# Kernel tuning notes

Measured on AMD Instinct MI355X. Metric: run time of the kernel, lower is better.

Reference implementation:

```python
import jax, jax.numpy as jnp
import numpy as np

N = 50000
E = 800000
IN_C = 256
OUT_C = 256
HEADS = 8
HEAD_C = OUT_C // HEADS  # 32
BNECK = OUT_C // 4       # 64
NEG_SLOPE = 0.2
BN_EPS = 1e-5


def _bn(x, gamma, beta):
    # BatchNorm1d over node dim, batch statistics (deterministic train-mode math)
    mu = jnp.mean(x, axis=0)
    var = jnp.var(x, axis=0)
    return (x - mu) * jax.lax.rsqrt(var + BN_EPS) * gamma + beta


def setup_inputs() -> dict:
    key = jax.random.key(0)
    ks = jax.random.split(key, 16)
    s = lambda fan: 1.0 / np.sqrt(fan)
    x = jax.random.normal(ks[0], (N, IN_C), dtype=jnp.float32)
    edge_index = jax.random.randint(ks[1], (2, E), 0, N, dtype=jnp.int64)
    return {
        "x": x,
        "edge_index": edge_index,
        # GATConv params (lin has no bias in PyG)
        "W_lin": jax.random.normal(ks[2], (IN_C, HEADS * HEAD_C), jnp.float32) * s(IN_C),
        "att_src": jax.random.normal(ks[3], (HEADS, HEAD_C), jnp.float32) * s(HEAD_C),
        "att_dst": jax.random.normal(ks[4], (HEADS, HEAD_C), jnp.float32) * s(HEAD_C),
        "conv_bias": jnp.zeros((HEADS * HEAD_C,), jnp.float32),
        "W_res": jax.random.normal(ks[5], (IN_C, HEADS * HEAD_C), jnp.float32) * s(IN_C),
        # gnn.BatchNorm
        "g_norm": jnp.ones((OUT_C,), jnp.float32),
        "b_norm": jnp.zeros((OUT_C,), jnp.float32),
        # Bottleneck down
        "W_down": jax.random.normal(ks[6], (OUT_C, BNECK), jnp.float32) * s(OUT_C),
        "b_down": jnp.zeros((BNECK,), jnp.float32),
        "g_down": jnp.ones((BNECK,), jnp.float32),
        "bb_down": jnp.zeros((BNECK,), jnp.float32),
        # Bottleneck up
        "W_up": jax.random.normal(ks[7], (BNECK, OUT_C), jnp.float32) * s(BNECK),
        "b_up": jnp.zeros((OUT_C,), jnp.float32),
        "g_up": jnp.ones((OUT_C,), jnp.float32),
        "bb_up": jnp.zeros((OUT_C,), jnp.float32),
    }


def _forward(x, edge_index, W_lin, att_src, att_dst, conv_bias, W_res,
             g_norm, b_norm, W_down, b_down, g_down, bb_down,
             W_up, b_up, g_up, bb_up):
    src, dst = edge_index[0], edge_index[1]
    # --- GATConv ---
    xh = (x @ W_lin).reshape(N, HEADS, HEAD_C)            # [N,H,C]
    a_src = jnp.einsum("nhc,hc->nh", xh, att_src)          # [N,H]
    a_dst = jnp.einsum("nhc,hc->nh", xh, att_dst)          # [N,H]
    e = a_src[src] + a_dst[dst]                             # [E,H]
    e = jnp.where(e > 0, e, NEG_SLOPE * e)                  # leaky_relu
    # segment softmax over destination nodes (numerically stable)
    m = jax.ops.segment_max(e, dst, num_segments=N)         # [N,H]
    m = jnp.where(jnp.isfinite(m), m, 0.0)
    ex = jnp.exp(e - m[dst])
    denom = jax.ops.segment_sum(ex, dst, num_segments=N)    # [N,H]
    alpha = ex / (denom[dst] + 1e-16)                        # [E,H]
    msgs = xh[src] * alpha[:, :, None]                       # [E,H,C]
    out = jax.ops.segment_sum(msgs, dst, num_segments=N)    # [N,H,C]
    out = out.reshape(N, HEADS * HEAD_C) + conv_bias + x @ W_res  # GAT residual + bias
    # --- norm + act ---
    h = jax.nn.elu(_bn(out, g_norm, b_norm))
    # --- bottleneck ---
    d = jax.nn.elu(_bn(h @ W_down + b_down, g_down, bb_down))
    u = jax.nn.elu(_bn(d @ W_up + b_up, g_up, bb_up))
    h = h + u
    # dropout: eval mode (identity); in==out so identity skip
    return h + x


def reference(x, edge_index, W_lin, att_src, att_dst, conv_bias, W_res,
              g_norm, b_norm, W_down, b_down, g_down, bb_down,
              W_up, b_up, g_up, bb_up):
    return _forward(x, edge_index, W_lin, att_src, att_dst, conv_bias, W_res,
                    g_norm, b_norm, W_down, b_down, g_down, bb_down,
                    W_up, b_up, g_up, bb_up)
```

## Files before the change

### kernel.cpp

```cpp
#include <hip/hip_runtime.h>

#define NN 50000
#define EE 800000
#define HEADS 8
#define NEG 0.2f
#define BN_EPS 1e-5f
#define SCAN_B 196
#define STAT_B 64

typedef unsigned int uint;
typedef unsigned short ushort;

typedef __bf16 bf16x8 __attribute__((ext_vector_type(8)));
typedef float f32x4 __attribute__((ext_vector_type(4)));

__device__ __forceinline__ float bflo(uint u) { return __uint_as_float(u << 16); }
__device__ __forceinline__ float bfhi(uint u) { return __uint_as_float(u & 0xffff0000u); }
__device__ __forceinline__ float bf1(ushort u) { return __uint_as_float(((uint)u) << 16); }
__device__ __forceinline__ ushort f2bf(float f) {
  uint u = __float_as_uint(f);
  u += 0x7fff + ((u >> 16) & 1);
  return (ushort)(u >> 16);
}
__device__ __forceinline__ uint pk2(float a, float b) {
  return (uint)f2bf(a) | ((uint)f2bf(b) << 16);
}
__device__ __forceinline__ float eluf(float v) { return v > 0.f ? v : expm1f(v); }

__global__ void k_detect(const uint* __restrict__ xw, const int* __restrict__ ew,
                         int* __restrict__ flags) {
  int l = threadIdx.x;
  int good = 0, zeros = 0;
#pragma unroll
  for (int j = 0; j < 4; ++j) {
    uint lo = xw[l * 4 + j] & 0xffffu;
    uint ex = (lo >> 7) & 0xffu;
    good += (ex >= 110u && ex <= 140u) ? 1 : 0;
    zeros += (ew[2 * (l * 4 + j) + 1] == 0) ? 1 : 0;
  }
  for (int o = 32; o; o >>= 1) { good += __shfl_down(good, o); zeros += __shfl_down(zeros, o); }
  if (l == 0) { flags[0] = (good >= 128) ? 1 : 0; flags[1] = (zeros >= 200) ? 1 : 0; }
}

__global__ void k_params(const void* p0, const void* p1, const void* p2, const void* p3,
                         const void* p4, const void* p5, const void* p6, const void* p7,
                         const void* p8, const void* p9, const void* p10,
                         float* __restrict__ P, const int* __restrict__ flags) {
  const void* srcs[11] = {p0, p1, p2, p3, p4, p5, p6, p7, p8, p9, p10};
  const int sz[11]  = {256, 256, 256, 256, 256, 64, 64, 64, 256, 256, 256};
  const int off[11] = {0, 256, 512, 768, 1024, 1280, 1344, 1408, 1472, 1728, 1984};
  int b = blockIdx.x, t = threadIdx.x;
  if (t < sz[b]) {
    const void* s = srcs[b];
    float v = flags[0] ? bf1(((const ushort*)s)[t]) : ((const float*)s)[t];
    P[off[b] + t] = v;
  }
}

__global__ void k_transpose(const void* __restrict__ src, ushort* __restrict__ dst,
                            int R, int C, int D, const int* __restrict__ flags) {
  __shared__ ushort tile[64][65];
  int r0 = blockIdx.x * 64, c0 = blockIdx.y * 64;
  int t = threadIdx.x;
  int tr = t >> 6;
  int tc = t & 63;
  int bf = flags[0];
#pragma unroll
  for (int i = 0; i < 16; ++i) {
    int rl = tr + i * 4;
    int r = r0 + rl, c = c0 + tc;
    float v = 0.f;
    if (r < R && c < C)
      v = bf ? bf1(((const ushort*)src)[(size_t)r * C + c])
             : ((const float*)src)[(size_t)r * C + c];
    tile[rl][tc] = f2bf(v);
  }
  __syncthreads();
#pragma unroll
  for (int i = 0; i < 16; ++i) {
    int cl = tr + i * 4;
    int rl = tc;
    int c = c0 + cl, r = r0 + rl;
    if (c < D && r < R)
      dst[(size_t)c * R + r] = (c < C) ? tile[rl][cl] : (ushort)0;
  }
}

__global__ void k_edges(const int* __restrict__ raw, int* __restrict__ sc, int* __restrict__ dc,
                        int* __restrict__ count, const int* __restrict__ flags) {
  int e = blockIdx.x * 256 + threadIdx.x;
  if (e >= EE) return;
  int s, d;
  if (flags[1]) { s = raw[2 * e]; d = raw[2 * (EE + e)]; }
  else          { s = raw[e];     d = raw[EE + e]; }
  if ((uint)s >= NN) s = 0;
  if ((uint)d >= NN) d = 0;
  sc[e] = s; dc[e] = d;
  atomicAdd(&count[d], 1);
}

__global__ __launch_bounds__(256)
void k_gemm(const void* __restrict__ A, const ushort* __restrict__ Bt,
            const int* __restrict__ flags, int aMode,
            int M, int K, int mode,
            ushort* __restrict__ o_xh, ushort* __restrict__ o_xres,
            ushort* __restrict__ o_bf, int NC, const float* __restrict__ bias) {
  __shared__ __align__(16) ushort As[128 * 32];
  __shared__ __align__(16) ushort Bs[128 * 32];
  int t = threadIdx.x;
  int l = t & 63, w = t >> 6;
  int wr = w >> 1, wc = w & 1;
  int lr = l & 15, lq = l >> 4;
  int m0 = blockIdx.y * 128;
  int n0 = blockIdx.x * 128;
  const int af32 = (aMode == 1) && (flags[0] == 0);
  const ushort* Ab = (const ushort*)A;
  const float*  Af = (const float*)A;

  f32x4 acc[4][4];
#pragma unroll
  for (int i = 0; i < 4; ++i)
#pragma unroll
    for (int j = 0; j < 4; ++j) acc[i][j] = (f32x4){0.f, 0.f, 0.f, 0.f};

  for (int kt = 0; kt < K; kt += 32) {
    __syncthreads();
#pragma unroll
    for (int r = 0; r < 2; ++r) {
      int ci = r * 256 + t;
      int m = ci >> 2, ko = (ci & 3) << 3;
      int gm = m0 + m; gm = gm < M ? gm : M - 1;
      if (af32) {
        float4 u0 = *(const float4*)(Af + (size_t)gm * K + kt + ko);
        float4 u1 = *(const float4*)(Af + (size_t)gm * K + kt + ko + 4);
        uint4 o;
        o.x = pk2(u0.x, u0.y); o.y = pk2(u0.z, u0.w);
        o.z = pk2(u1.x, u1.y); o.w = pk2(u1.z, u1.w);
        *(uint4*)(&As[m * 32 + ko]) = o;
      } else {
        *(uint4*)(&As[m * 32 + ko]) = *(const uint4*)(Ab + (size_t)gm * K + kt + ko);
      }
      *(uint4*)(&Bs[m * 32 + ko]) = *(const uint4*)(Bt + (size_t)(n0 + m) * K + kt + ko);
    }
    __syncthreads();
    bf16x8 af[4], bf[4];
#pragma unroll
    for (int i = 0; i < 4; ++i) {
      af[i] = *(const bf16x8*)(&As[(wr * 64 + i * 16 + lr) * 32 + lq * 8]);
      bf[i] = *(const bf16x8*)(&Bs[(wc * 64 + i * 16 + lr) * 32 + lq * 8]);
    }
#pragma unroll
    for (int i = 0; i < 4; ++i)
#pragma unroll
      for (int j = 0; j < 4; ++j)
        acc[i][j] = __builtin_amdgcn_mfma_f32_16x16x32_bf16(af[i], bf[j], acc[i][j], 0, 0, 0);
  }

#pragma unroll
  for (int i = 0; i < 4; ++i) {
    int gr0 = m0 + wr * 64 + i * 16 + lq * 4;
#pragma unroll
    for (int j = 0; j < 4; ++j) {
      int gc = n0 + wc * 64 + j * 16 + lr;
#pragma unroll
      for (int r = 0; r < 4; ++r) {
        int row = gr0 + r;
        if (row >= M) continue;
        float v = acc[i][j][r];
        if (mode == 0) {
          if (gc < 256) o_xh[(size_t)row * 256 + gc] = f2bf(v);
          else          o_xres[(size_t)row * 256 + (gc - 256)] = f2bf(v);
        } else {
          if (gc < NC) o_bf[(size_t)row * NC + gc] = f2bf(v + bias[gc]);
        }
      }
    }
  }
}

__global__ void k_attn(const ushort* __restrict__ xh, const float* __restrict__ P,
                       float* __restrict__ a_src, float* __restrict__ a_dst) {
  int id = blockIdx.x * 256 + threadIdx.x;
  if (id >= NN * HEADS) return;
  int n = id >> 3, h = id & 7;
  const uint4* xr = (const uint4*)(xh + (size_t)n * 256 + h * 32);
  const float4* pa = (const float4*)(P + h * 32);
  const float4* pd = (const float4*)(P + 256 + h * 32);
  float s = 0.f, d = 0.f;
#pragma unroll
  for (int j = 0; j < 4; ++j) {
    uint4 q = xr[j];
    float4 a0 = pa[2 * j], a1 = pa[2 * j + 1];
    float4 d0 = pd[2 * j], d1 = pd[2 * j + 1];
    float x0 = bflo(q.x), x1 = bfhi(q.x), x2 = bflo(q.y), x3 = bfhi(q.y);
    float x4 = bflo(q.z), x5 = bfhi(q.z), x6 = bflo(q.w), x7 = bfhi(q.w);
    s += x0 * a0.x + x1 * a0.y + x2 * a0.z + x3 * a0.w
       + x4 * a1.x + x5 * a1.y + x6 * a1.z + x7 * a1.w;
    d += x0 * d0.x + x1 * d0.y + x2 * d0.z + x3 * d0.w
       + x4 * d1.x + x5 * d1.y + x6 * d1.z + x7 * d1.w;
  }
  a_src[id] = s; a_dst[id] = d;
}

__global__ void k_scan_bs(const int* __restrict__ count, int* __restrict__ bsum) {
  __shared__ int s[256];
  int i = blockIdx.x * 256 + threadIdx.x;
  s[threadIdx.x] = (i < NN) ? count[i] : 0;
  __syncthreads();
  for (int off = 128; off > 0; off >>= 1) {
    if (threadIdx.x < off) s[threadIdx.x] += s[threadIdx.x + off];
    __syncthreads();
  }
  if (threadIdx.x == 0) bsum[blockIdx.x] = s[0];
}

__global__ void k_scan_top(const int* __restrict__ bsum, int* __restrict__ boff,
                           int* __restrict__ rowptr) {
  __shared__ int s[256];
  int t = threadIdx.x;
  int v = (t < SCAN_B) ? bsum[t] : 0;
  s[t] = v;
  __syncthreads();
  for (int off = 1; off < 256; off <<= 1) {
    int u = (t >= off) ? s[t - off] : 0;
    __syncthreads();
    s[t] += u;
    __syncthreads();
  }
  boff[t] = s[t] - v;
  if (t == 255) rowptr[NN] = s[255];
}

__global__ void k_scan_wr(const int* __restrict__ count, const int* __restrict__ boff,
                          int* __restrict__ rowptr, int* __restrict__ rowwork) {
  __shared__ int s[256];
  int b = blockIdx.x, t = threadIdx.x;
  int i = b * 256 + t;
  int v = (i < NN) ? count[i] : 0;
  s[t] = v;
  __syncthreads();
  for (int off = 1; off < 256; off <<= 1) {
    int u = (t >= off) ? s[t - off] : 0;
    __syncthreads();
    s[t] += u;
    __syncthreads();
  }
  if (i < NN) {
    int ex = boff[b] + s[t] - v;
    rowptr[i] = ex;
    rowwork[i] = ex;
  }
}

__global__ void k_scatter(const int* __restrict__ sc, const int* __restrict__ dc,
                          int* __restrict__ rowwork, int* __restrict__ perm_src) {
  int e = blockIdx.x * 256 + threadIdx.x;
  if (e >= EE) return;
  int pos = atomicAdd(&rowwork[dc[e]], 1);
  perm_src[pos] = sc[e];
}

__global__ __launch_bounds__(256)
void k_aggregate(const int* __restrict__ rowptr, const int* __restrict__ perm_src,
                 const float* __restrict__ a_src, const float* __restrict__ a_dst,
                 const ushort* __restrict__ xh, const ushort* __restrict__ xres,
                 const float* __restrict__ bias, ushort* __restrict__ outb) {
  int n = blockIdx.x * 4 + (threadIdx.x >> 6);
  int l = threadIdx.x & 63;
  if (n >= NN) return;
  int half = l >> 5;
  int q = l & 31;
  int h = q >> 2;
  float ad = a_dst[n * 8 + h];
  int st = rowptr[n], en = rowptr[n + 1];
  float a0 = 0.f, a1 = 0.f, a2 = 0.f, a3 = 0.f;
  float a4 = 0.f, a5 = 0.f, a6 = 0.f, a7 = 0.f, sum = 0.f;
  int p = st + half;
  int s_c = 0; float e_c = 0.f; uint4 x_c = {0, 0, 0, 0};
  if (p < en) {
    s_c = perm_src[p];
    e_c = a_src[s_c * 8 + h];
    x_c = *(const uint4*)(xh + (size_t)s_c * 256 + q * 8);
  }
  for (; p < en; p += 2) {
    int pn = p + 2;
    int s_n = 0; float e_n = 0.f; uint4 x_n = {0, 0, 0, 0};
    if (pn < en) {
      s_n = perm_src[pn];
      e_n = a_src[s_n * 8 + h];
      x_n = *(const uint4*)(xh + (size_t)s_n * 256 + q * 8);
    }
    float v = e_c + ad;
    v = v > 0.f ? v : NEG * v;
    float wgt = __expf(fminf(v, 60.f));
    sum += wgt;
    a0 += wgt * bflo(x_c.x); a1 += wgt * bfhi(x_c.x);
    a2 += wgt * bflo(x_c.y); a3 += wgt * bfhi(x_c.y);
    a4 += wgt * bflo(x_c.z); a5 += wgt * bfhi(x_c.z);
    a6 += wgt * bflo(x_c.w); a7 += wgt * bfhi(x_c.w);
    s_c = s_n; e_c = e_n; x_c = x_n;
  }
  sum += __shfl_xor(sum, 32);
  a0 += __shfl_xor(a0, 32); a1 += __shfl_xor(a1, 32);
  a2 += __shfl_xor(a2, 32); a3 += __shfl_xor(a3, 32);
  a4 += __shfl_xor(a4, 32); a5 += __shfl_xor(a5, 32);
  a6 += __shfl_xor(a6, 32); a7 += __shfl_xor(a7, 32);
  if (half == 0) {
    float inv = 1.0f / (sum + 1e-16f);
    int cb = q * 8;
    float4 b0 = *(const float4*)(bias + cb);
    float4 b1 = *(const float4*)(bias + cb + 4);
    uint4 qr = *(const uint4*)(xres + (size_t)n * 256 + cb);
    uint4 pk;
    pk.x = pk2(a0 * inv + b0.x + bflo(qr.x), a1 * inv + b0.y + bfhi(qr.x));
    pk.y = pk2(a2 * inv + b0.z + bflo(qr.y), a3 * inv + b0.w + bfhi(qr.y));
    pk.z = pk2(a4 * inv + b1.x + bflo(qr.z), a5 * inv + b1.y + bfhi(qr.z));
    pk.w = pk2(a6 * inv + b1.z + bflo(qr.w), a7 * inv + b1.w + bfhi(qr.w));
    *(uint4*)(outb + (size_t)n * 256 + cb) = pk;
  }
}

__global__ __launch_bounds__(256)
void k_stats_p(const ushort* __restrict__ x, float* __restrict__ partial, int n, int C) {
  __shared__ float4 redA[256];
  __shared__ float4 redB[256];
  int t = threadIdx.x, b = blockIdx.x;
  int W = C >> 2;
  int c4 = t & (W - 1);
  int rl = t / W;
  int G = 256 / W;
  int rows = (n + STAT_B - 1) / STAT_B;
  int r0 = b * rows, r1 = r0 + rows; if (r1 > n) r1 = n;
  const uint2* xu = (const uint2*)x;
  float s0 = 0, s1 = 0, s2 = 0, s3 = 0, q0 = 0, q1 = 0, q2 = 0, q3 = 0;
  for (int r = r0 + rl; r < r1; r += G) {
    uint2 v = xu[(size_t)r * W + c4];
    float v0 = bflo(v.x), v1 = bfhi(v.x), v2 = bflo(v.y), v3 = bfhi(v.y);
    s0 += v0; s1 += v1; s2 += v2; s3 += v3;
    q0 += v0 * v0; q1 += v1 * v1; q2 += v2 * v2; q3 += v3 * v3;
  }
  redA[t] = make_float4(s0, s1, s2, s3);
  redB[t] = make_float4(q0, q1, q2, q3);
  __syncthreads();
  for (int off = 128; off >= W; off >>= 1) {
    if (t < off) {
      float4 a = redA[t + off], c = redA[t];
      redA[t] = make_float4(c.x + a.x, c.y + a.y, c.z + a.z, c.w + a.w);
      float4 d = redB[t + off], e = redB[t];
      redB[t] = make_float4(e.x + d.x, e.y + d.y, e.z + d.z, e.w + d.w);
    }
    __syncthreads();
  }
  if (t < W) {
    float4 a = redA[t], d = redB[t];
    float* ps = partial + (size_t)b * 2 * C;
    ps[4 * c4 + 0] = a.x; ps[4 * c4 + 1] = a.y;
    ps[4 * c4 + 2] = a.z; ps[4 * c4 + 3] = a.w;
    ps[C + 4 * c4 + 0] = d.x; ps[C + 4 * c4 + 1] = d.y;
    ps[C + 4 * c4 + 2] = d.z; ps[C + 4 * c4 + 3] = d.w;
  }
}

__global__ void k_stats_r(const float* __restrict__ partial, float* __restrict__ sums, int C2) {
  int c = blockIdx.x * 256 + threadIdx.x;
  if (c >= C2) return;
  float s = 0.f;
  for (int b = 0; b < STAT_B; ++b) s += partial[(size_t)b * C2 + c];
  sums[c] = s;
}

__global__ void k_bnact1(const ushort* __restrict__ xin, const float* __restrict__ sums,
                         const float* __restrict__ g, const float* __restrict__ b,
                         ushort* __restrict__ h1b) {
  int id = blockIdx.x * 256 + threadIdx.x;
  size_t base = (size_t)id * 4;
  if (base >= (size_t)NN * 256) return;
  int c = (int)(base & 255);
  const float invN = 1.0f / NN;
  float4 sm = *(const float4*)(sums + c);
  float4 sq = *(const float4*)(sums + 256 + c);
  float4 g4 = *(const float4*)(g + c);
  float4 b4 = *(const float4*)(b + c);
  uint2 qv = *(const uint2*)(xin + base);
  float vv[4] = {bflo(qv.x), bfhi(qv.x), bflo(qv.y), bfhi(qv.y)};
  float smv[4] = {sm.x, sm.y, sm.z, sm.w}, sqv[4] = {sq.x, sq.y, sq.z, sq.w};
  float gv[4] = {g4.x, g4.y, g4.z, g4.w}, bv[4] = {b4.x, b4.y, b4.z, b4.w};
  float o[4];
#pragma unroll
  for (int j = 0; j < 4; ++j) {
    float mean = smv[j] * invN;
    float var = sqv[j] * invN - mean * mean;
    float sc = gv[j] * rsqrtf(var + BN_EPS);
    o[j] = eluf((vv[j] - mean) * sc + bv[j]);
  }
  uint2 pk;
  pk.x = pk2(o[0], o[1]);
  pk.y = pk2(o[2], o[3]);
  *(uint2*)(h1b + base) = pk;
}

__global__ void k_bnact2(const ushort* __restrict__ xin, const float* __restrict__ sums,
                         const float* __restrict__ g, const float* __restrict__ b,
                         ushort* __restrict__ db) {
  int id = blockIdx.x * 256 + threadIdx.x;
  size_t base = (size_t)id * 4;
  if (base >= (size_t)NN * 64) return;
  int c = (int)(base & 63);
  const float invN = 1.0f / NN;
  float4 sm = *(const float4*)(sums + c);
  float4 sq = *(const float4*)(sums + 64 + c);
  float4 g4 = *(const float4*)(g + c);
  float4 b4 = *(const float4*)(b + c);
  uint2 qv = *(const uint2*)(xin + base);
  float vv[4] = {bflo(qv.x), bfhi(qv.x), bflo(qv.y), bfhi(qv.y)};
  float smv[4] = {sm.x, sm.y, sm.z, sm.w}, sqv[4] = {sq.x, sq.y, sq.z, sq.w};
  float gv[4] = {g4.x, g4.y, g4.z, g4.w}, bv[4] = {b4.x, b4.y, b4.z, b4.w};
  float o[4];
#pragma unroll
  for (int j = 0; j < 4; ++j) {
    float mean = smv[j] * invN;
    float var = sqv[j] * invN - mean * mean;
    float sc = gv[j] * rsqrtf(var + BN_EPS);
    o[j] = eluf((vv[j] - mean) * sc + bv[j]);
  }
  uint2 pk;
  pk.x = pk2(o[0], o[1]);
  pk.y = pk2(o[2], o[3]);
  *(uint2*)(db + base) = pk;
}

__global__ void k_final(const ushort* __restrict__ upre, const float* __restrict__ sums,
                        const float* __restrict__ g, const float* __restrict__ b,
                        const ushort* __restrict__ h1b, const void* __restrict__ xsrc,
                        void* __restrict__ outv, const int* __restrict__ flags) {
  int id = blockIdx.x * 256 + threadIdx.x;
  size_t base = (size_t)id * 4;
  if (base >= (size_t)NN * 256) return;
  int c = (int)(base & 255);
  const float invN = 1.0f / NN;
  float4 sm = *(const float4*)(sums + c);
  float4 sq = *(const float4*)(sums + 256 + c);
  float4 g4 = *(const float4*)(g + c);
  float4 b4 = *(const float4*)(b + c);
  uint2 qv = *(const uint2*)(upre + base);
  uint2 qh = *(const uint2*)(h1b + base);
  float xv[4];
  if (flags[0]) {
    uint2 qx = *(const uint2*)((const ushort*)xsrc + base);
    xv[0] = bflo(qx.x); xv[1] = bfhi(qx.x); xv[2] = bflo(qx.y); xv[3] = bfhi(qx.y);
  } else {
    float4 qx = *(const float4*)((const float*)xsrc + base);
    xv[0] = qx.x; xv[1] = qx.y; xv[2] = qx.z; xv[3] = qx.w;
  }
  float vv[4] = {bflo(qv.x), bfhi(qv.x), bflo(qv.y), bfhi(qv.y)};
  float hv[4] = {bflo(qh.x), bfhi(qh.x), bflo(qh.y), bfhi(qh.y)};
  float smv[4] = {sm.x, sm.y, sm.z, sm.w}, sqv[4] = {sq.x, sq.y, sq.z, sq.w};
  float gv[4] = {g4.x, g4.y, g4.z, g4.w}, bv[4] = {b4.x, b4.y, b4.z, b4.w};
  float o[4];
#pragma unroll
  for (int j = 0; j < 4; ++j) {
    float mean = smv[j] * invN;
    float var = sqv[j] * invN - mean * mean;
    float sc = gv[j] * rsqrtf(var + BN_EPS);
    o[j] = eluf((vv[j] - mean) * sc + bv[j]) + hv[j] + xv[j];
  }
  if (flags[0]) {
    uint2 pk;
    pk.x = pk2(o[0], o[1]);
    pk.y = pk2(o[2], o[3]);
    *(uint2*)((ushort*)outv + base) = pk;
  } else {
    *(float4*)((float*)outv + base) = make_float4(o[0], o[1], o[2], o[3]);
  }
}

extern "C" void kernel_launch(void* const* d_in, const int* in_sizes, int n_in,
                              void* d_out, int out_size, void* d_ws, size_t ws_size,
                              hipStream_t stream) {
  const void* x      = d_in[0];
  const int*  ei     = (const int*)d_in[1];
  const void* W_lin  = d_in[2];
  const void* att_s  = d_in[3];
  const void* att_d  = d_in[4];
  const void* c_bias = d_in[5];
  const void* W_res  = d_in[6];
  const void* g_norm = d_in[7];
  const void* b_norm = d_in[8];
  const void* W_down = d_in[9];
  const void* b_down = d_in[10];
  const void* g_down = d_in[11];
  const void* bb_down= d_in[12];
  const void* W_up   = d_in[13];
  const void* b_up   = d_in[14];
  const void* g_up   = d_in[15];
  const void* bb_up  = d_in[16];

  char* ws = (char*)d_ws;
  size_t off = 0;
  auto alloc = [&](size_t bytes) -> char* {
    char* p = ws + off;
    off = (off + bytes + 255) & ~(size_t)255;
    return p;
  };
  int*   flags  = (int*)alloc(2 * 4);
  int*   count  = (int*)alloc((size_t)NN * 4);
  size_t zbytes = off;
  float* sums1  = (float*)alloc(512 * 4);
  float* sums2  = (float*)alloc(128 * 4);
  float* sums3  = (float*)alloc(512 * 4);
  float* partial= (float*)alloc((size_t)STAT_B * 512 * 4);
  float* P      = (float*)alloc(2240 * 4);
  int* bsum     = (int*)alloc(256 * 4);
  int* boff     = (int*)alloc(256 * 4);
  int* rowptr   = (int*)alloc((size_t)(NN + 1) * 4);
  int* rowwork  = (int*)alloc((size_t)(NN + 1) * 4);
  int* src_c    = (int*)alloc((size_t)EE * 4);
  int* dst_c    = (int*)alloc((size_t)EE * 4);
  int* perm_src = (int*)alloc((size_t)EE * 4);
  ushort* bt1   = (ushort*)alloc((size_t)512 * 256 * 2);
  ushort* bt2   = (ushort*)alloc((size_t)128 * 256 * 2);
  ushort* bt3   = (ushort*)alloc((size_t)256 * 64 * 2);
  float* a_src  = (float*)alloc((size_t)NN * 8 * 4);
  float* a_dst  = (float*)alloc((size_t)NN * 8 * 4);
  ushort* xh    = (ushort*)alloc((size_t)NN * 256 * 2);
  ushort* xres  = (ushort*)alloc((size_t)NN * 256 * 2);
  ushort* og_b  = (ushort*)alloc((size_t)NN * 256 * 2);
  ushort* d_b   = (ushort*)alloc((size_t)NN * 64 * 2);
  ushort* h1b    = xres;
  ushort* d_pre_b= xh;
  ushort* u_pre_b= og_b;

  hipMemsetAsync(d_ws, 0, zbytes, stream);

  hipLaunchKernelGGL(k_detect, dim3(1), dim3(64), 0, stream, (const uint*)x, ei, flags);
  hipLaunchKernelGGL(k_params, dim3(11), dim3(256), 0, stream,
                     att_s, att_d, c_bias, g_norm, b_norm, b_down, g_down, bb_down,
                     b_up, g_up, bb_up, P, flags);
  hipLaunchKernelGGL(k_transpose, dim3(4, 4), dim3(256), 0, stream, W_lin, bt1, 256, 256, 256, flags);
  hipLaunchKernelGGL(k_transpose, dim3(4, 4), dim3(256), 0, stream, W_res, bt1 + 256 * 256, 256, 256, 256, flags);
  hipLaunchKernelGGL(k_transpose, dim3(4, 2), dim3(256), 0, stream, W_down, bt2, 256, 64, 128, flags);
  hipLaunchKernelGGL(k_transpose, dim3(1, 4), dim3(256), 0, stream, W_up, bt3, 64, 256, 256, flags);
  hipLaunchKernelGGL(k_edges, dim3((EE + 255) / 256), dim3(256), 0, stream,
                     ei, src_c, dst_c, count, flags);

  hipLaunchKernelGGL(k_gemm, dim3(4, 391), dim3(256), 0, stream, x, bt1, flags, 1,
                     NN, 256, 0, xh, xres, (ushort*)nullptr, 0, (const float*)nullptr);
  hipLaunchKernelGGL(k_attn, dim3((NN * 8 + 255) / 256), dim3(256), 0, stream,
                     xh, P, a_src, a_dst);

  hipLaunchKernelGGL(k_scan_bs, dim3(SCAN_B), dim3(256), 0, stream, count, bsum);
  hipLaunchKernelGGL(k_scan_top, dim3(1), dim3(256), 0, stream, bsum, boff, rowptr);
  hipLaunchKernelGGL(k_scan_wr, dim3(SCAN_B), dim3(256), 0, stream, count, boff, rowptr, rowwork);
  hipLaunchKernelGGL(k_scatter, dim3((EE + 255) / 256), dim3(256), 0, stream,
                     src_c, dst_c, rowwork, perm_src);

  hipLaunchKernelGGL(k_aggregate, dim3(NN / 4), dim3(256), 0, stream, rowptr, perm_src,
                     a_src, a_dst, xh, xres, P + 512, og_b);

  hipLaunchKernelGGL(k_stats_p, dim3(STAT_B), dim3(256), 0, stream, og_b, partial, NN, 256);
  hipLaunchKernelGGL(k_stats_r, dim3(2), dim3(256), 0, stream, partial, sums1, 512);
  hipLaunchKernelGGL(k_bnact1, dim3(NN * 256 / 4 / 256), dim3(256), 0, stream,
                     og_b, sums1, P + 768, P + 1024, h1b);

  hipLaunchKernelGGL(k_gemm, dim3(1, 391), dim3(256), 0, stream, h1b, bt2, flags, 0,
                     NN, 256, 1, (ushort*)nullptr, (ushort*)nullptr, d_pre_b, 64, P + 1280);
  hipLaunchKernelGGL(k_stats_p, dim3(STAT_B), dim3(256), 0, stream, d_pre_b, partial, NN, 64);
  hipLaunchKernelGGL(k_stats_r, dim3(1), dim3(256), 0, stream, partial, sums2, 128);
  hipLaunchKernelGGL(k_bnact2, dim3(NN * 64 / 4 / 256), dim3(256), 0, stream,
                     d_pre_b, sums2, P + 1344, P + 1408, d_b);

  hipLaunchKernelGGL(k_gemm, dim3(2, 391), dim3(256), 0, stream, d_b, bt3, flags, 0,
                     NN, 64, 1, (ushort*)nullptr, (ushort*)nullptr, u_pre_b, 256, P + 1472);
  hipLaunchKernelGGL(k_stats_p, dim3(STAT_B), dim3(256), 0, stream, u_pre_b, partial, NN, 256);
  hipLaunchKernelGGL(k_stats_r, dim3(2), dim3(256), 0, stream, partial, sums3, 512);
  hipLaunchKernelGGL(k_final, dim3(NN * 256 / 4 / 256), dim3(256), 0, stream,
                     u_pre_b, sums3, P + 1728, P + 1984, h1b, x, d_out, flags);
}
```

Baseline: 613.6 us.

## Fuse BN+ELU into GEMM A-load, merge prep kernels, atomic stats reduction

```diff
diff --git a/kernel.cpp b/kernel.cpp
--- a/kernel.cpp
+++ b/kernel.cpp
@@ -6,7 +6,6 @@
 #define NEG 0.2f
 #define BN_EPS 1e-5f
 #define SCAN_B 196
-#define STAT_B 64
 
 typedef unsigned int uint;
 typedef unsigned short ushort;
@@ -27,44 +26,67 @@
 }
 __device__ __forceinline__ float eluf(float v) { return v > 0.f ? v : expm1f(v); }
 
-__global__ void k_detect(const uint* __restrict__ xw, const int* __restrict__ ew,
-                         int* __restrict__ flags) {
-  int l = threadIdx.x;
-  int good = 0, zeros = 0;
-#pragma unroll
-  for (int j = 0; j < 4; ++j) {
-    uint lo = xw[l * 4 + j] & 0xffffu;
-    uint ex = (lo >> 7) & 0xffu;
-    good += (ex >= 110u && ex <= 140u) ? 1 : 0;
-    zeros += (ew[2 * (l * 4 + j) + 1] == 0) ? 1 : 0;
-  }
-  for (int o = 32; o; o >>= 1) { good += __shfl_down(good, o); zeros += __shfl_down(zeros, o); }
-  if (l == 0) { flags[0] = (good >= 128) ? 1 : 0; flags[1] = (zeros >= 200) ? 1 : 0; }
-}
-
-__global__ void k_params(const void* p0, const void* p1, const void* p2, const void* p3,
-                         const void* p4, const void* p5, const void* p6, const void* p7,
-                         const void* p8, const void* p9, const void* p10,
-                         float* __restrict__ P, const int* __restrict__ flags) {
-  const void* srcs[11] = {p0, p1, p2, p3, p4, p5, p6, p7, p8, p9, p10};
-  const int sz[11]  = {256, 256, 256, 256, 256, 64, 64, 64, 256, 256, 256};
-  const int off[11] = {0, 256, 512, 768, 1024, 1280, 1344, 1408, 1472, 1728, 1984};
+__device__ __forceinline__ int blk_detect_bf16(const uint* __restrict__ xw) {
+  __shared__ int s_bf;
+  int t = threadIdx.x;
+  if (t < 64) {
+    int good = 0;
+#pragma unroll
+    for (int j = 0; j < 4; ++j) {
+      uint lo = xw[t * 4 + j] & 0xffffu;
+      uint ex = (lo >> 7) & 0xffu;
+      good += (ex >= 110u && ex <= 140u) ? 1 : 0;
+    }
+    for (int o = 32; o; o >>= 1) good += __shfl_down(good, o);
+    if (t == 0) s_bf = (good >= 128) ? 1 : 0;
+  }
+  __syncthreads();
+  return s_bf;
+}
+
+__device__ __forceinline__ int blk_detect_i64(const int* __restrict__ ew) {
+  __shared__ int s_i64;
+  int t = threadIdx.x;
+  if (t < 64) {
+    int zeros = 0;
+#pragma unroll
+    for (int j = 0; j < 4; ++j)
+      zeros += (ew[2 * (t * 4 + j) + 1] == 0) ? 1 : 0;
+    for (int o = 32; o; o >>= 1) zeros += __shfl_down(zeros, o);
+    if (t == 0) s_i64 = (zeros >= 200) ? 1 : 0;
+  }
+  __syncthreads();
+  return s_i64;
+}
+
+__global__ __launch_bounds__(256)
+void k_prep(const void* __restrict__ x,
+            const void* p0, const void* p1, const void* p2, const void* p3,
+            const void* p4, const void* p5, const void* p6, const void* p7,
+            const void* p8, const void* p9, const void* p10,
+            const void* W_lin, const void* W_res, const void* W_down, const void* W_up,
+            float* __restrict__ P, ushort* __restrict__ bt1,
+            ushort* __restrict__ bt2, ushort* __restrict__ bt3) {
+  __shared__ ushort tile[64][65];
+  int bf = blk_detect_bf16((const uint*)x);
   int b = blockIdx.x, t = threadIdx.x;
-  if (t < sz[b]) {
-    const void* s = srcs[b];
-    float v = flags[0] ? bf1(((const ushort*)s)[t]) : ((const float*)s)[t];
-    P[off[b] + t] = v;
-  }
-}
-
-__global__ void k_transpose(const void* __restrict__ src, ushort* __restrict__ dst,
-                            int R, int C, int D, const int* __restrict__ flags) {
-  __shared__ ushort tile[64][65];
-  int r0 = blockIdx.x * 64, c0 = blockIdx.y * 64;
-  int t = threadIdx.x;
-  int tr = t >> 6;
-  int tc = t & 63;
-  int bf = flags[0];
+  if (b < 11) {
+    const void* srcs[11] = {p0, p1, p2, p3, p4, p5, p6, p7, p8, p9, p10};
+    const int sz[11]  = {256, 256, 256, 256, 256, 64, 64, 64, 256, 256, 256};
+    const int off[11] = {0, 256, 512, 768, 1024, 1280, 1344, 1408, 1472, 1728, 1984};
+    if (t < sz[b]) {
+      const void* s = srcs[b];
+      P[off[b] + t] = bf ? bf1(((const ushort*)s)[t]) : ((const float*)s)[t];
+    }
+    return;
+  }
+  const void* src; ushort* dst; int R, C, D, rb, cb;
+  if (b < 27)      { int u = b - 11; src = W_lin;  dst = bt1;         R = 256; C = 256; D = 256; rb = u & 3; cb = u >> 2; }
+  else if (b < 43) { int u = b - 27; src = W_res;  dst = bt1 + 65536; R = 256; C = 256; D = 256; rb = u & 3; cb = u >> 2; }
+  else if (b < 51) { int u = b - 43; src = W_down; dst = bt2;         R = 256; C = 64;  D = 128; rb = u & 3; cb = u >> 2; }
+  else             { int u = b - 51; src = W_up;   dst = bt3;         R = 64;  C = 256; D = 256; rb = 0;     cb = u; }
+  int r0 = rb * 64, c0 = cb * 64;
+  int tr = t >> 6, tc = t & 63;
 #pragma unroll
   for (int i = 0; i < 16; ++i) {
     int rl = tr + i * 4;
@@ -86,13 +108,15 @@
   }
 }
 
-__global__ void k_edges(const int* __restrict__ raw, int* __restrict__ sc, int* __restrict__ dc,
-                        int* __restrict__ count, const int* __restrict__ flags) {
+__global__ __launch_bounds__(256)
+void k_edges(const int* __restrict__ raw, int* __restrict__ sc, int* __restrict__ dc,
+             int* __restrict__ count) {
+  int i64 = blk_detect_i64(raw);
   int e = blockIdx.x * 256 + threadIdx.x;
   if (e >= EE) return;
   int s, d;
-  if (flags[1]) { s = raw[2 * e]; d = raw[2 * (EE + e)]; }
-  else          { s = raw[e];     d = raw[EE + e]; }
+  if (i64) { s = raw[2 * e]; d = raw[2 * (EE + e)]; }
+  else     { s = raw[e];     d = raw[EE + e]; }
   if ((uint)s >= NN) s = 0;
   if ((uint)d >= NN) d = 0;
   sc[e] = s; dc[e] = d;
@@ -101,77 +125,108 @@
 
 __global__ __launch_bounds__(256)
 void k_gemm(const void* __restrict__ A, const ushort* __restrict__ Bt,
-            const int* __restrict__ flags, int aMode,
-            int M, int K, int mode,
+            int aMode, int nIter, int M, int K, int mode,
             ushort* __restrict__ o_xh, ushort* __restrict__ o_xres,
-            ushort* __restrict__ o_bf, int NC, const float* __restrict__ bias) {
+            ushort* __restrict__ o_bf, int NC, const float* __restrict__ bias,
+            const float* __restrict__ bnsums, const float* __restrict__ bng,
+            const float* __restrict__ bnb) {
   __shared__ __align__(16) ushort As[128 * 32];
   __shared__ __align__(16) ushort Bs[128 * 32];
+  __shared__ float scs[256], shs[256];
   int t = threadIdx.x;
   int l = t & 63, w = t >> 6;
   int wr = w >> 1, wc = w & 1;
   int lr = l & 15, lq = l >> 4;
-  int m0 = blockIdx.y * 128;
-  int n0 = blockIdx.x * 128;
-  const int af32 = (aMode == 1) && (flags[0] == 0);
+  int m0 = blockIdx.x * 128;
   const ushort* Ab = (const ushort*)A;
   const float*  Af = (const float*)A;
 
-  f32x4 acc[4][4];
-#pragma unroll
-  for (int i = 0; i < 4; ++i)
-#pragma unroll
-    for (int j = 0; j < 4; ++j) acc[i][j] = (f32x4){0.f, 0.f, 0.f, 0.f};
-
-  for (int kt = 0; kt < K; kt += 32) {
-    __syncthreads();
-#pragma unroll
-    for (int r = 0; r < 2; ++r) {
-      int ci = r * 256 + t;
-      int m = ci >> 2, ko = (ci & 3) << 3;
-      int gm = m0 + m; gm = gm < M ? gm : M - 1;
-      if (af32) {
-        float4 u0 = *(const float4*)(Af + (size_t)gm * K + kt + ko);
-        float4 u1 = *(const float4*)(Af + (size_t)gm * K + kt + ko + 4);
-        uint4 o;
-        o.x = pk2(u0.x, u0.y); o.y = pk2(u0.z, u0.w);
-        o.z = pk2(u1.x, u1.y); o.w = pk2(u1.z, u1.w);
-        *(uint4*)(&As[m * 32 + ko]) = o;
-      } else {
-        *(uint4*)(&As[m * 32 + ko]) = *(const uint4*)(Ab + (size_t)gm * K + kt + ko);
+  int af32 = 0;
+  if (aMode == 1) af32 = blk_detect_bf16((const uint*)A) ? 0 : 1;
+  if (aMode == 2) {
+    if (t < K) {
+      const float invN = 1.0f / NN;
+      float mean = bnsums[t] * invN;
+      float var = bnsums[K + t] * invN - mean * mean;
+      float sc = bng[t] * rsqrtf(var + BN_EPS);
+      scs[t] = sc;
+      shs[t] = bnb[t] - mean * sc;
+    }
+  }
+
+  for (int nc = 0; nc < nIter; ++nc) {
+    int n0 = nc * 128;
+    f32x4 acc[4][4];
+#pragma unroll
+    for (int i = 0; i < 4; ++i)
+#pragma unroll
+      for (int j = 0; j < 4; ++j) acc[i][j] = (f32x4){0.f, 0.f, 0.f, 0.f};
+
+    for (int kt = 0; kt < K; kt += 32) {
+      __syncthreads();
+#pragma unroll
+      for (int r = 0; r < 2; ++r) {
+        int ci = r * 256 + t;
+        int m = ci >> 2, ko = (ci & 3) << 3;
+        int gm = m0 + m; gm = gm < M ? gm : M - 1;
+        if (aMode == 1 && af32) {
+          float4 u0 = *(const float4*)(Af + (size_t)gm * K + kt + ko);
+          float4 u1 = *(const float4*)(Af + (size_t)gm * K + kt + ko + 4);
+          uint4 o;
+          o.x = pk2(u0.x, u0.y); o.y = pk2(u0.z, u0.w);
+          o.z = pk2(u1.x, u1.y); o.w = pk2(u1.z, u1.w);
+          *(uint4*)(&As[m * 32 + ko]) = o;
+        } else if (aMode == 2) {
+          uint4 q = *(const uint4*)(Ab + (size_t)gm * K + kt + ko);
+          int cb = kt + ko;
+          float v0 = eluf(bflo(q.x) * scs[cb + 0] + shs[cb + 0]);
+          float v1 = eluf(bfhi(q.x) * scs[cb + 1] + shs[cb + 1]);
+          float v2 = eluf(bflo(q.y) * scs[cb + 2] + shs[cb + 2]);
+          float v3 = eluf(bfhi(q.y) * scs[cb + 3] + shs[cb + 3]);
+          float v4 = eluf(bflo(q.z) * scs[cb + 4] + shs[cb + 4]);
+          float v5 = eluf(bfhi(q.z) * scs[cb + 5] + shs[cb + 5]);
+          float v6 = eluf(bflo(q.w) * scs[cb + 6] + shs[cb + 6]);
+          float v7 = eluf(bfhi(q.w) * scs[cb + 7] + shs[cb + 7]);
+          uint4 o;
+          o.x = pk2(v0, v1); o.y = pk2(v2, v3);
+          o.z = pk2(v4, v5); o.w = pk2(v6, v7);
+          *(uint4*)(&As[m * 32 + ko]) = o;
+        } else {
+          *(uint4*)(&As[m * 32 + ko]) = *(const uint4*)(Ab + (size_t)gm * K + kt + ko);
+        }
+        *(uint4*)(&Bs[m * 32 + ko]) = *(const uint4*)(Bt + (size_t)(n0 + m) * K + kt + ko);
       }
-      *(uint4*)(&Bs[m * 32 + ko]) = *(const uint4*)(Bt + (size_t)(n0 + m) * K + kt + ko);
-    }
-    __syncthreads();
-    bf16x8 af[4], bf[4];
+      __syncthreads();
+      bf16x8 af[4], bf[4];
+#pragma unroll
+      for (int i = 0; i < 4; ++i) {
+        af[i] = *(const bf16x8*)(&As[(wr * 64 + i * 16 + lr) * 32 + lq * 8]);
+        bf[i] = *(const bf16x8*)(&Bs[(wc * 64 + i * 16 + lr) * 32 + lq * 8]);
+      }
+#pragma unroll
+      for (int i = 0; i < 4; ++i)
+#pragma unroll
+        for (int j = 0; j < 4; ++j)
+          acc[i][j] = __builtin_amdgcn_mfma_f32_16x16x32_bf16(af[i], bf[j], acc[i][j], 0, 0, 0);
+    }
+
 #pragma unroll
     for (int i = 0; i < 4; ++i) {
-      af[i] = *(const bf16x8*)(&As[(wr * 64 + i * 16 + lr) * 32 + lq * 8]);
-      bf[i] = *(const bf16x8*)(&Bs[(wc * 64 + i * 16 + lr) * 32 + lq * 8]);
-    }
-#pragma unroll
-    for (int i = 0; i < 4; ++i)
-#pragma unroll
-      for (int j = 0; j < 4; ++j)
-        acc[i][j] = __builtin_amdgcn_mfma_f32_16x16x32_bf16(af[i], bf[j], acc[i][j], 0, 0, 0);
-  }
-
-#pragma unroll
-  for (int i = 0; i < 4; ++i) {
-    int gr0 = m0 + wr * 64 + i * 16 + lq * 4;
-#pragma unroll
-    for (int j = 0; j < 4; ++j) {
-      int gc = n0 + wc * 64 + j * 16 + lr;
-#pragma unroll
-      for (int r = 0; r < 4; ++r) {
-        int row = gr0 + r;
-        if (row >= M) continue;
-        float v = acc[i][j][r];
-        if (mode == 0) {
-          if (gc < 256) o_xh[(size_t)row * 256 + gc] = f2bf(v);
-          else          o_xres[(size_t)row * 256 + (gc - 256)] = f2bf(v);
-        } else {
-          if (gc < NC) o_bf[(size_t)row * NC + gc] = f2bf(v + bias[gc]);
+      int gr0 = m0 + wr * 64 + i * 16 + lq * 4;
+#pragma unroll
+      for (int j = 0; j < 4; ++j) {
+        int gc = n0 + wc * 64 + j * 16 + lr;
+#pragma unroll
+        for (int r = 0; r < 4; ++r) {
+          int row = gr0 + r;
+          if (row >= M) continue;
+          float v = acc[i][j][r];
+          if (mode == 0) {
+            if (gc < 256) o_xh[(size_t)row * 256 + gc] = f2bf(v);
+            else          o_xres[(size_t)row * 256 + (gc - 256)] = f2bf(v);
+          } else {
+            if (gc < NC) o_bf[(size_t)row * NC + gc] = f2bf(v + bias[gc]);
+          }
         }
       }
     }
@@ -321,7 +376,7 @@
 }
 
 __global__ __launch_bounds__(256)
-void k_stats_p(const ushort* __restrict__ x, float* __restrict__ partial, int n, int C) {
+void k_stats_p(const ushort* __restrict__ x, float* __restrict__ sums, int n, int C) {
   __shared__ float4 redA[256];
   __shared__ float4 redB[256];
   int t = threadIdx.x, b = blockIdx.x;
@@ -329,7 +384,7 @@
   int c4 = t & (W - 1);
   int rl = t / W;
   int G = 256 / W;
-  int rows = (n + STAT_B - 1) / STAT_B;
+  int rows = (n + 63) / 64;
   int r0 = b * rows, r1 = r0 + rows; if (r1 > n) r1 = n;
   const uint2* xu = (const uint2*)x;
   float s0 = 0, s1 = 0, s2 = 0, s3 = 0, q0 = 0, q1 = 0, q2 = 0, q3 = 0;
@@ -353,118 +408,61 @@
   }
   if (t < W) {
     float4 a = redA[t], d = redB[t];
-    float* ps = partial + (size_t)b * 2 * C;
-    ps[4 * c4 + 0] = a.x; ps[4 * c4 + 1] = a.y;
-    ps[4 * c4 + 2] = a.z; ps[4 * c4 + 3] = a.w;
-    ps[C + 4 * c4 + 0] = d.x; ps[C + 4 * c4 + 1] = d.y;
-    ps[C + 4 * c4 + 2] = d.z; ps[C + 4 * c4 + 3] = d.w;
-  }
-}
-
-__global__ void k_stats_r(const float* __restrict__ partial, float* __restrict__ sums, int C2) {
-  int c = blockIdx.x * 256 + threadIdx.x;
-  if (c >= C2) return;
-  float s = 0.f;
-  for (int b = 0; b < STAT_B; ++b) s += partial[(size_t)b * C2 + c];
-  sums[c] = s;
-}
-
-__global__ void k_bnact1(const ushort* __restrict__ xin, const float* __restrict__ sums,
-                         const float* __restrict__ g, const float* __restrict__ b,
-                         ushort* __restrict__ h1b) {
+    atomicAdd(&sums[4 * c4 + 0], a.x); atomicAdd(&sums[4 * c4 + 1], a.y);
+    atomicAdd(&sums[4 * c4 + 2], a.z); atomicAdd(&sums[4 * c4 + 3], a.w);
+    atomicAdd(&sums[C + 4 * c4 + 0], d.x); atomicAdd(&sums[C + 4 * c4 + 1], d.y);
+    atomicAdd(&sums[C + 4 * c4 + 2], d.z); atomicAdd(&sums[C + 4 * c4 + 3], d.w);
+  }
+}
+
+__global__ void k_final(const ushort* __restrict__ upre, const float* __restrict__ sums3,
+                        const ushort* __restrict__ og, const float* __restrict__ sums1,
+                        const float* __restrict__ P, const void* __restrict__ xsrc,
+                        void* __restrict__ outv) {
+  int bf = blk_detect_bf16((const uint*)xsrc);
   int id = blockIdx.x * 256 + threadIdx.x;
   size_t base = (size_t)id * 4;
   if (base >= (size_t)NN * 256) return;
   int c = (int)(base & 255);
   const float invN = 1.0f / NN;
-  float4 sm = *(const float4*)(sums + c);
-  float4 sq = *(const float4*)(sums + 256 + c);
-  float4 g4 = *(const float4*)(g + c);
-  float4 b4 = *(const float4*)(b + c);
-  uint2 qv = *(const uint2*)(xin + base);
-  float vv[4] = {bflo(qv.x), bfhi(qv.x), bflo(qv.y), bfhi(qv.y)};
-  float smv[4] = {sm.x, sm.y, sm.z, sm.w}, sqv[4] = {sq.x, sq.y, sq.z, sq.w};
-  float gv[4] = {g4.x, g4.y, g4.z, g4.w}, bv[4] = {b4.x, b4.y, b4.z, b4.w};
-  float o[4];
-#pragma unroll
-  for (int j = 0; j < 4; ++j) {
-    float mean = smv[j] * invN;
-    float var = sqv[j] * invN - mean * mean;
-    float sc = gv[j] * rsqrtf(var + BN_EPS);
-    o[j] = eluf((vv[j] - mean) * sc + bv[j]);
-  }
-  uint2 pk;
-  pk.x = pk2(o[0], o[1]);
-  pk.y = pk2(o[2], o[3]);
-  *(uint2*)(h1b + base) = pk;
-}
-
-__global__ void k_bnact2(const ushort* __restrict__ xin, const float* __restrict__ sums,
-                         const float* __restrict__ g, const float* __restrict__ b,
-                         ushort* __restrict__ db) {
-  int id = blockIdx.x * 256 + threadIdx.x;
-  size_t base = (size_t)id * 4;
-  if (base >= (size_t)NN * 64) return;
-  int c = (int)(base & 63);
-  const float invN = 1.0f / NN;
-  float4 sm = *(const float4*)(sums + c);
-  float4 sq = *(const float4*)(sums + 64 + c);
-  float4 g4 = *(const float4*)(g + c);
-  float4 b4 = *(const float4*)(b + c);
-  uint2 qv = *(const uint2*)(xin + base);
-  float vv[4] = {bflo(qv.x), bfhi(qv.x), bflo(qv.y), bfhi(qv.y)};
-  float smv[4] = {sm.x, sm.y, sm.z, sm.w}, sqv[4] = {sq.x, sq.y, sq.z, sq.w};
-  float gv[4] = {g4.x, g4.y, g4.z, g4.w}, bv[4] = {b4.x, b4.y, b4.z, b4.w};
-  float o[4];
-#pragma unroll
-  for (int j = 0; j < 4; ++j) {
-    float mean = smv[j] * invN;
-    float var = sqv[j] * invN - mean * mean;
-    float sc = gv[j] * rsqrtf(var + BN_EPS);
-    o[j] = eluf((vv[j] - mean) * sc + bv[j]);
-  }
-  uint2 pk;
-  pk.x = pk2(o[0], o[1]);
-  pk.y = pk2(o[2], o[3]);
-  *(uint2*)(db + base) = pk;
-}
-
-__global__ void k_final(const ushort* __restrict__ upre, const float* __restrict__ sums,
-                        const float* __restrict__ g, const float* __restrict__ b,
-                        const ushort* __restrict__ h1b, const void* __restrict__ xsrc,
-                        void* __restrict__ outv, const int* __restrict__ flags) {
-  int id = blockIdx.x * 256 + threadIdx.x;
-  size_t base = (size_t)id * 4;
-  if (base >= (size_t)NN * 256) return;
-  int c = (int)(base & 255);
-  const float invN = 1.0f / NN;
-  float4 sm = *(const float4*)(sums + c);
-  float4 sq = *(const float4*)(sums + 256 + c);
-  float4 g4 = *(const float4*)(g + c);
-  float4 b4 = *(const float4*)(b + c);
-  uint2 qv = *(const uint2*)(upre + base);
-  uint2 qh = *(const uint2*)(h1b + base);
+  float4 s3m = *(const float4*)(sums3 + c);
+  float4 s3q = *(const float4*)(sums3 + 256 + c);
+  float4 g3 = *(const float4*)(P + 1728 + c);
+  float4 b3 = *(const float4*)(P + 1984 + c);
+  float4 s1m = *(const float4*)(sums1 + c);
+  float4 s1q = *(const float4*)(sums1 + 256 + c);
+  float4 g1 = *(const float4*)(P + 768 + c);
+  float4 b1 = *(const float4*)(P + 1024 + c);
+  uint2 qu = *(const uint2*)(upre + base);
+  uint2 qo = *(const uint2*)(og + base);
   float xv[4];
-  if (flags[0]) {
+  if (bf) {
     uint2 qx = *(const uint2*)((const ushort*)xsrc + base);
     xv[0] = bflo(qx.x); xv[1] = bfhi(qx.x); xv[2] = bflo(qx.y); xv[3] = bfhi(qx.y);
   } else {
     float4 qx = *(const float4*)((const float*)xsrc + base);
     xv[0] = qx.x; xv[1] = qx.y; xv[2] = qx.z; xv[3] = qx.w;
   }
-  float vv[4] = {bflo(qv.x), bfhi(qv.x), bflo(qv.y), bfhi(qv.y)};
-  float hv[4] = {bflo(qh.x), bfhi(qh.x), bflo(qh.y), bfhi(qh.y)};
-  float smv[4] = {sm.x, sm.y, sm.z, sm.w}, sqv[4] = {sq.x, sq.y, sq.z, sq.w};
-  float gv[4] = {g4.x, g4.y, g4.z, g4.w}, bv[4] = {b4.x, b4.y, b4.z, b4.w};
+  float uv[4] = {bflo(qu.x), bfhi(qu.x), bflo(qu.y), bfhi(qu.y)};
+  float ov[4] = {bflo(qo.x), bfhi(qo.x), bflo(qo.y), bfhi(qo.y)};
+  float s3mv[4] = {s3m.x, s3m.y, s3m.z, s3m.w}, s3qv[4] = {s3q.x, s3q.y, s3q.z, s3q.w};
+  float g3v[4] = {g3.x, g3.y, g3.z, g3.w}, b3v[4] = {b3.x, b3.y, b3.z, b3.w};
+  float s1mv[4] = {s1m.x, s1m.y, s1m.z, s1m.w}, s1qv[4] = {s1q.x, s1q.y, s1q.z, s1q.w};
+  float g1v[4] = {g1.x, g1.y, g1.z, g1.w}, b1v[4] = {b1.x, b1.y, b1.z, b1.w};
   float o[4];
 #pragma unroll
   for (int j = 0; j < 4; ++j) {
-    float mean = smv[j] * invN;
-    float var = sqv[j] * invN - mean * mean;
-    float sc = gv[j] * rsqrtf(var + BN_EPS);
-    o[j] = eluf((vv[j] - mean) * sc + bv[j]) + hv[j] + xv[j];
-  }
-  if (flags[0]) {
+    float m3 = s3mv[j] * invN;
+    float v3 = s3qv[j] * invN - m3 * m3;
+    float sc3 = g3v[j] * rsqrtf(v3 + BN_EPS);
+    float u = eluf((uv[j] - m3) * sc3 + b3v[j]);
+    float m1 = s1mv[j] * invN;
+    float v1 = s1qv[j] * invN - m1 * m1;
+    float sc1 = g1v[j] * rsqrtf(v1 + BN_EPS);
+    float h1 = eluf((ov[j] - m1) * sc1 + b1v[j]);
+    o[j] = u + h1 + xv[j];
+  }
+  if (bf) {
     uint2 pk;
     pk.x = pk2(o[0], o[1]);
     pk.y = pk2(o[2], o[3]);
@@ -502,13 +500,11 @@
     off = (off + bytes + 255) & ~(size_t)255;
     return p;
   };
-  int*   flags  = (int*)alloc(2 * 4);
   int*   count  = (int*)alloc((size_t)NN * 4);
-  size_t zbytes = off;
   float* sums1  = (float*)alloc(512 * 4);
   float* sums2  = (float*)alloc(128 * 4);
   float* sums3  = (float*)alloc(512 * 4);
-  float* partial= (float*)alloc((size_t)STAT_B * 512 * 4);
+  size_t zbytes = off;
   float* P      = (float*)alloc(2240 * 4);
   int* bsum     = (int*)alloc(256 * 4);
   int* boff     = (int*)alloc(256 * 4);
@@ -525,26 +521,21 @@
   ushort* xh    = (ushort*)alloc((size_t)NN * 256 * 2);
   ushort* xres  = (ushort*)alloc((size_t)NN * 256 * 2);
   ushort* og_b  = (ushort*)alloc((size_t)NN * 256 * 2);
-  ushort* d_b   = (ushort*)alloc((size_t)NN * 64 * 2);
-  ushort* h1b    = xres;
-  ushort* d_pre_b= xh;
-  ushort* u_pre_b= og_b;
+  ushort* d_pre_b = xh;
+  ushort* u_pre_b = xres;
 
   hipMemsetAsync(d_ws, 0, zbytes, stream);
 
-  hipLaunchKernelGGL(k_detect, dim3(1), dim3(64), 0, stream, (const uint*)x, ei, flags);
-  hipLaunchKernelGGL(k_params, dim3(11), dim3(256), 0, stream,
+  hipLaunchKernelGGL(k_prep, dim3(55), dim3(256), 0, stream, x,
                      att_s, att_d, c_bias, g_norm, b_norm, b_down, g_down, bb_down,
-                     b_up, g_up, bb_up, P, flags);
-  hipLaunchKernelGGL(k_transpose, dim3(4, 4), dim3(256), 0, stream, W_lin, bt1, 256, 256, 256, flags);
-  hipLaunchKernelGGL(k_transpose, dim3(4, 4), dim3(256), 0, stream, W_res, bt1 + 256 * 256, 256, 256, 256, flags);
-  hipLaunchKernelGGL(k_transpose, dim3(4, 2), dim3(256), 0, stream, W_down, bt2, 256, 64, 128, flags);
-  hipLaunchKernelGGL(k_transpose, dim3(1, 4), dim3(256), 0, stream, W_up, bt3, 64, 256, 256, flags);
+                     b_up, g_up, bb_up, W_lin, W_res, W_down, W_up, P, bt1, bt2, bt3);
   hipLaunchKernelGGL(k_edges, dim3((EE + 255) / 256), dim3(256), 0, stream,
-                     ei, src_c, dst_c, count, flags);
-
-  hipLaunchKernelGGL(k_gemm, dim3(4, 391), dim3(256), 0, stream, x, bt1, flags, 1,
-                     NN, 256, 0, xh, xres, (ushort*)nullptr, 0, (const float*)nullptr);
+                     ei, src_c, dst_c, count);
+
+  hipLaunchKernelGGL(k_gemm, dim3(391), dim3(256), 0, stream, x, bt1, 1, 4,
+                     NN, 256, 0, xh, xres, (ushort*)nullptr, 0,
+                     (const float*)nullptr, (const float*)nullptr,
+                     (const float*)nullptr, (const float*)nullptr);
   hipLaunchKernelGGL(k_attn, dim3((NN * 8 + 255) / 256), dim3(256), 0, stream,
                      xh, P, a_src, a_dst);
 
@@ -557,22 +548,18 @@
   hipLaunchKernelGGL(k_aggregate, dim3(NN / 4), dim3(256), 0, stream, rowptr, perm_src,
                      a_src, a_dst, xh, xres, P + 512, og_b);
 
-  hipLaunchKernelGGL(k_stats_p, dim3(STAT_B), dim3(256), 0, stream, og_b, partial, NN, 256);
-  hipLaunchKernelGGL(k_stats_r, dim3(2), dim3(256), 0, stream, partial, sums1, 512);
-  hipLaunchKernelGGL(k_bnact1, dim3(NN * 256 / 4 / 256), dim3(256), 0, stream,
-                     og_b, sums1, P + 768, P + 1024, h1b);
-
-  hipLaunchKernelGGL(k_gemm, dim3(1, 391), dim3(256), 0, stream, h1b, bt2, flags, 0,
-                     NN, 256, 1, (ushort*)nullptr, (ushort*)nullptr, d_pre_b, 64, P + 1280);
-  hipLaunchKernelGGL(k_stats_p, dim3(STAT_B), dim3(256), 0, stream, d_pre_b, partial, NN, 64);
-  hipLaunchKernelGGL(k_stats_r, dim3(1), dim3(256), 0, stream, partial, sums2, 128);
-  hipLaunchKernelGGL(k_bnact2, dim3(NN * 64 / 4 / 256), dim3(256), 0, stream,
-                     d_pre_b, sums2, P + 1344, P + 1408, d_b);
-
-  hipLaunchKernelGGL(k_gemm, dim3(2, 391), dim3(256), 0, stream, d_b, bt3, flags, 0,
-                     NN, 64, 1, (ushort*)nullptr, (ushort*)nullptr, u_pre_b, 256, P + 1472);
-  hipLaunchKernelGGL(k_stats_p, dim3(STAT_B), dim3(256), 0, stream, u_pre_b, partial, NN, 256);
-  hipLaunchKernelGGL(k_stats_r, dim3(2), dim3(256), 0, stream, partial, sums3, 512);
+  hipLaunchKernelGGL(k_stats_p, dim3(64), dim3(256), 0, stream, og_b, sums1, NN, 256);
+
+  hipLaunchKernelGGL(k_gemm, dim3(391), dim3(256), 0, stream, og_b, bt2, 2, 1,
+                     NN, 256, 1, (ushort*)nullptr, (ushort*)nullptr, d_pre_b, 64,
+                     P + 1280, sums1, P + 768, P + 1024);
+  hipLaunchKernelGGL(k_stats_p, dim3(64), dim3(256), 0, stream, d_pre_b, sums2, NN, 64);
+
+  hipLaunchKernelGGL(k_gemm, dim3(391), dim3(256), 0, stream, d_pre_b, bt3, 2, 2,
+                     NN, 64, 1, (ushort*)nullptr, (ushort*)nullptr, u_pre_b, 256,
+                     P + 1472, sums2, P + 1344, P + 1408);
+  hipLaunchKernelGGL(k_stats_p, dim3(64), dim3(256), 0, stream, u_pre_b, sums3, NN, 256);
+
   hipLaunchKernelGGL(k_final, dim3(NN * 256 / 4 / 256), dim3(256), 0, stream,
-                     u_pre_b, sums3, P + 1728, P + 1984, h1b, x, d_out, flags);
-}
+                     u_pre_b, sums3, og_b, sums1, P, x, d_out);
+}
```

Measured after the change: 621.3 us. No clear change (+1.3%).
